# Kernel optimization log

Hardware: AMD Instinct MI355X
Metric: run time of the kernel (lower is better)

The kernel has to match this reference:

```python
import jax, jax.numpy as jnp
import numpy as np

WINDOW_SIZE = 11
SIGMA = 1.5
COLOR_TRANS = np.array([65.738, 129.057, 25.064], dtype=np.float32)
C1 = (0.01 * 255) ** 2
C2 = (0.03 * 255) ** 2


def _make_window(ws=WINDOW_SIZE, sigma=SIGMA):
    x = np.arange(ws, dtype=np.float32)
    g = np.exp(-((x - ws // 2) ** 2) / (2.0 * sigma ** 2))
    g = g / g.sum()
    w2d = np.outer(g, g).astype(np.float32)  # [ws, ws]
    return jnp.asarray(w2d[None, None])      # [1,1,ws,ws] OIHW


def _conv(x, w):
    # x: [B,1,H,W], w: [1,1,ws,ws], VALID padding, single channel
    return jax.lax.conv_general_dilated(
        x, w, window_strides=(1, 1), padding='VALID',
        dimension_numbers=('NCHW', 'OIHW', 'NCHW'))


def _luma(img):
    # img: [B,H,W,>=3] in [-1,1] -> [B,1,H,W] luma in [16,235]-ish
    rgb = (img[..., :3] + 1.0) / 2.0 * 255.0
    y = jnp.matmul(rgb, jnp.asarray(COLOR_TRANS)) / 256.0 + 16.0
    return y[:, None, :, :]


def setup_inputs() -> dict:
    key = jax.random.key(0)
    k1, k2 = jax.random.split(key)
    shape = (32, 512, 512, 3)
    img1 = jax.random.uniform(k1, shape, jnp.float32, -1.0, 1.0)
    img2 = jax.random.uniform(k2, shape, jnp.float32, -1.0, 1.0)
    return {"img1": img1, "img2": img2}


def reference(img1, img2):
    w = _make_window()
    x1 = _luma(img1)
    x2 = _luma(img2)
    mu1 = _conv(x1, w)
    mu2 = _conv(x2, w)
    mu1_sq = mu1 * mu1
    mu2_sq = mu2 * mu2
    mu1_mu2 = mu1 * mu2
    sigma1_sq = _conv(x1 * x1, w) - mu1_sq
    sigma2_sq = _conv(x2 * x2, w) - mu2_sq
    sigma12 = _conv(x1 * x2, w) - mu1_mu2
    ssim_map = ((2 * mu1_mu2 + C1) * (2 * sigma12 + C2)) / (
        (mu1_sq + mu2_sq + C1) * (sigma1_sq + sigma2_sq + C2))
    return jnp.mean(ssim_map)
```

## Files before the change

kernel.cpp:

```cpp
#include <hip/hip_runtime.h>
#include <math.h>

#define BATCH 32
#define H 512
#define W 512
#define OUTD 502
#define WS 11
#define TX 32
#define TY 32
#define IX 42
#define IY 42

#define C1F 6.5025f
#define C2F 58.5225f
#define N_OUT_TOTAL 8064128.0

struct GW { float g[WS]; };

__global__ __launch_bounds__(256) void ssim_tile_kernel(
    const float* __restrict__ img1, const float* __restrict__ img2,
    double* __restrict__ acc, GW w)
{
    __shared__ float sA[IY][IX + 2];
    __shared__ float sB[IY][IX + 2];
    __shared__ float hc[5][IY][TX + 1];
    __shared__ double wsum[4];

    const int tid  = threadIdx.x;
    const int c0   = blockIdx.x * TX;
    const int r0   = blockIdx.y * TY;
    const int b    = blockIdx.z;

    {
        const int tx = tid & 63;
        const int ty = tid >> 6;
        if (tx < IX) {
            const int col = c0 + tx;
            for (int iy = ty; iy < IY; iy += 4) {
                const int row = r0 + iy;
                float la = 0.f, lb = 0.f;
                if (row < H && col < W) {
                    const size_t base = ((size_t)(b * H + row) * W + col) * 3;
                    float r1 = img1[base], g1 = img1[base + 1], b1 = img1[base + 2];
                    float r2 = img2[base], g2 = img2[base + 1], b2 = img2[base + 2];
                    r1 = (r1 + 1.f) * 127.5f; g1 = (g1 + 1.f) * 127.5f; b1 = (b1 + 1.f) * 127.5f;
                    r2 = (r2 + 1.f) * 127.5f; g2 = (g2 + 1.f) * 127.5f; b2 = (b2 + 1.f) * 127.5f;
                    la = (r1 * 65.738f + g1 * 129.057f + b1 * 25.064f) * (1.f / 256.f) + 16.f;
                    lb = (r2 * 65.738f + g2 * 129.057f + b2 * 25.064f) * (1.f / 256.f) + 16.f;
                }
                sA[iy][tx] = la;
                sB[iy][tx] = lb;
            }
        }
    }
    __syncthreads();

    {
        const int ox = tid & 31;
        const int ty = tid >> 5;
        for (int iy = ty; iy < IY; iy += 8) {
            float s0 = 0.f, s1 = 0.f, s2 = 0.f, s3 = 0.f, s4 = 0.f;
            #pragma unroll
            for (int k = 0; k < WS; ++k) {
                const float gk = w.g[k];
                const float a = sA[iy][ox + k];
                const float c = sB[iy][ox + k];
                s0 += gk * a;
                s1 += gk * c;
                s2 += gk * a * a;
                s3 += gk * c * c;
                s4 += gk * a * c;
            }
            hc[0][iy][ox] = s0;
            hc[1][iy][ox] = s1;
            hc[2][iy][ox] = s2;
            hc[3][iy][ox] = s3;
            hc[4][iy][ox] = s4;
        }
    }
    __syncthreads();

    double local = 0.0;
    {
        const int ox = tid & 31;
        const int ty = tid >> 5;
        const bool col_ok = (c0 + ox) < OUTD;
        for (int oy = ty; oy < TY; oy += 8) {
            if (col_ok && (r0 + oy) < OUTD) {
                float mu1 = 0.f, mu2 = 0.f, e11 = 0.f, e22 = 0.f, e12 = 0.f;
                #pragma unroll
                for (int k = 0; k < WS; ++k) {
                    const float gk = w.g[k];
                    mu1 += gk * hc[0][oy + k][ox];
                    mu2 += gk * hc[1][oy + k][ox];
                    e11 += gk * hc[2][oy + k][ox];
                    e22 += gk * hc[3][oy + k][ox];
                    e12 += gk * hc[4][oy + k][ox];
                }
                const float mu1s = mu1 * mu1;
                const float mu2s = mu2 * mu2;
                const float mu12 = mu1 * mu2;
                const float s1q = e11 - mu1s;
                const float s2q = e22 - mu2s;
                const float s12 = e12 - mu12;
                const float num = (2.f * mu12 + C1F) * (2.f * s12 + C2F);
                const float den = (mu1s + mu2s + C1F) * (s1q + s2q + C2F);
                local += (double)(num / den);
            }
        }
    }

    for (int off = 32; off > 0; off >>= 1)
        local += __shfl_down(local, off, 64);
    const int lane = tid & 63;
    const int wv   = tid >> 6;
    if (lane == 0) wsum[wv] = local;
    __syncthreads();
    if (tid == 0) {
        const double t = wsum[0] + wsum[1] + wsum[2] + wsum[3];
        atomicAdd(acc, t);
    }
}

__global__ void ssim_finalize_kernel(const double* __restrict__ acc,
                                     float* __restrict__ out)
{
    out[0] = (float)(acc[0] / N_OUT_TOTAL);
}

extern "C" void kernel_launch(void* const* d_in, const int* in_sizes, int n_in,
                              void* d_out, int out_size, void* d_ws, size_t ws_size,
                              hipStream_t stream) {
    const float* img1 = (const float*)d_in[0];
    const float* img2 = (const float*)d_in[1];
    float* out = (float*)d_out;
    double* acc = (double*)d_ws;

    GW w;
    {
        float g[WS];
        float s = 0.f;
        for (int i = 0; i < WS; ++i) {
            const float x = (float)(i - WS / 2);
            g[i] = expf(-(x * x) / (2.f * 1.5f * 1.5f));
            s += g[i];
        }
        for (int i = 0; i < WS; ++i) w.g[i] = g[i] / s;
    }

    hipMemsetAsync(d_ws, 0, sizeof(double), stream);

    dim3 grid((OUTD + TX - 1) / TX, (OUTD + TY - 1) / TY, BATCH);
    ssim_tile_kernel<<<grid, 256, 0, stream>>>(img1, img2, acc, w);
    ssim_finalize_kernel<<<1, 1, 0, stream>>>(acc, out);
}
```

Measured before the change: 303.1 us.

## Stream rows through double-buffered LDS with register-resident vertical accumulators

Replaces the 32x32 2D tile kernel with a strip kernel where each thread owns one output column across a 32-row strip. Input rows are loaded one at a time into a double-buffered LDS row and prefetched a row ahead. The horizontal pass runs per row, and its result is scattered into an 11-deep ring of register accumulators for the vertical pass. This cuts the LDS footprint and the horizontal halo recompute (256-wide columns instead of 32). In exchange it adds a barrier per row, heavy register use (55 accumulators), and fewer blocks with wide column tiles.

```diff
diff --git a/kernel.cpp b/kernel.cpp
--- a/kernel.cpp
+++ b/kernel.cpp
@@ -6,119 +6,180 @@
 #define W 512
 #define OUTD 502
 #define WS 11
-#define TX 32
-#define TY 32
-#define IX 42
-#define IY 42
+#define STRIP 32
+#define INROWS 42
+#define BW 266
 
 #define C1F 6.5025f
 #define C2F 58.5225f
 #define N_OUT_TOTAL 8064128.0
 
 struct GW { float g[WS]; };
-
-__global__ __launch_bounds__(256) void ssim_tile_kernel(
+struct H5 { float v[5]; };
+
+__global__ __launch_bounds__(256, 4) void ssim_stream_kernel(
     const float* __restrict__ img1, const float* __restrict__ img2,
-    double* __restrict__ acc, GW w)
+    double* __restrict__ acc_out, GW wv)
 {
-    __shared__ float sA[IY][IX + 2];
-    __shared__ float sB[IY][IX + 2];
-    __shared__ float hc[5][IY][TX + 1];
+    __shared__ float bufA[2][BW];
+    __shared__ float bufB[2][BW];
     __shared__ double wsum[4];
 
-    const int tid  = threadIdx.x;
-    const int c0   = blockIdx.x * TX;
-    const int r0   = blockIdx.y * TY;
-    const int b    = blockIdx.z;
+    const int t  = threadIdx.x;
+    const int bx = blockIdx.x;
+    const int by = blockIdx.y;
+    const int b  = blockIdx.z;
+
+    const int c0   = bx * 256;
+    const int ox   = c0 + t;
+    const int r0   = by * STRIP;
+    const bool colok = (ox < OUTD);
+
+    const size_t imgbase = (size_t)b * H * W * 3;
+
+    auto load_luma = [&](int iy, float& la, float& lb, float& la2, float& lb2) {
+        la = lb = la2 = lb2 = 0.f;
+        const int r = r0 + iy;
+        if (iy < INROWS && r < H) {
+            const size_t rowb = imgbase + (size_t)r * (W * 3);
+            {
+                const size_t p = rowb + (size_t)(c0 + t) * 3;
+                float r1 = img1[p], g1 = img1[p + 1], b1 = img1[p + 2];
+                float r2 = img2[p], g2 = img2[p + 1], b2 = img2[p + 2];
+                r1 = (r1 + 1.f) * 127.5f; g1 = (g1 + 1.f) * 127.5f; b1 = (b1 + 1.f) * 127.5f;
+                r2 = (r2 + 1.f) * 127.5f; g2 = (g2 + 1.f) * 127.5f; b2 = (b2 + 1.f) * 127.5f;
+                la = (r1 * 65.738f + g1 * 129.057f + b1 * 25.064f) * (1.f / 256.f) + 16.f;
+                lb = (r2 * 65.738f + g2 * 129.057f + b2 * 25.064f) * (1.f / 256.f) + 16.f;
+            }
+            if (t < 10 && (c0 + 256 + t) < W) {
+                const size_t p = rowb + (size_t)(c0 + 256 + t) * 3;
+                float r1 = img1[p], g1 = img1[p + 1], b1 = img1[p + 2];
+                float r2 = img2[p], g2 = img2[p + 1], b2 = img2[p + 2];
+                r1 = (r1 + 1.f) * 127.5f; g1 = (g1 + 1.f) * 127.5f; b1 = (b1 + 1.f) * 127.5f;
+                r2 = (r2 + 1.f) * 127.5f; g2 = (g2 + 1.f) * 127.5f; b2 = (b2 + 1.f) * 127.5f;
+                la2 = (r1 * 65.738f + g1 * 129.057f + b1 * 25.064f) * (1.f / 256.f) + 16.f;
+                lb2 = (r2 * 65.738f + g2 * 129.057f + b2 * 25.064f) * (1.f / 256.f) + 16.f;
+            }
+        }
+    };
+
+    float rlA, rlB, rlA2, rlB2;
 
     {
-        const int tx = tid & 63;
-        const int ty = tid >> 6;
-        if (tx < IX) {
-            const int col = c0 + tx;
-            for (int iy = ty; iy < IY; iy += 4) {
-                const int row = r0 + iy;
-                float la = 0.f, lb = 0.f;
-                if (row < H && col < W) {
-                    const size_t base = ((size_t)(b * H + row) * W + col) * 3;
-                    float r1 = img1[base], g1 = img1[base + 1], b1 = img1[base + 2];
-                    float r2 = img2[base], g2 = img2[base + 1], b2 = img2[base + 2];
-                    r1 = (r1 + 1.f) * 127.5f; g1 = (g1 + 1.f) * 127.5f; b1 = (b1 + 1.f) * 127.5f;
-                    r2 = (r2 + 1.f) * 127.5f; g2 = (g2 + 1.f) * 127.5f; b2 = (b2 + 1.f) * 127.5f;
-                    la = (r1 * 65.738f + g1 * 129.057f + b1 * 25.064f) * (1.f / 256.f) + 16.f;
-                    lb = (r2 * 65.738f + g2 * 129.057f + b2 * 25.064f) * (1.f / 256.f) + 16.f;
-                }
-                sA[iy][tx] = la;
-                sB[iy][tx] = lb;
-            }
-        }
-    }
-    __syncthreads();
-
-    {
-        const int ox = tid & 31;
-        const int ty = tid >> 5;
-        for (int iy = ty; iy < IY; iy += 8) {
-            float s0 = 0.f, s1 = 0.f, s2 = 0.f, s3 = 0.f, s4 = 0.f;
+        float a, bv, a2, b2;
+        load_luma(0, a, bv, a2, b2);
+        load_luma(1, rlA, rlB, rlA2, rlB2);
+        bufA[0][t] = a; bufB[0][t] = bv;
+        if (t < 10) { bufA[0][256 + t] = a2; bufB[0][256 + t] = b2; }
+    }
+
+    auto row_step = [&](int iy) -> H5 {
+        float nA, nB, nA2, nB2;
+        load_luma(iy + 2, nA, nB, nA2, nB2);
+        __syncthreads();
+        {
+            const int wb = (iy + 1) & 1;
+            bufA[wb][t] = rlA; bufB[wb][t] = rlB;
+            if (t < 10) { bufA[wb][256 + t] = rlA2; bufB[wb][256 + t] = rlB2; }
+        }
+        rlA = nA; rlB = nB; rlA2 = nA2; rlB2 = nB2;
+        const float* __restrict__ ra = bufA[iy & 1];
+        const float* __restrict__ rb = bufB[iy & 1];
+        float h0 = 0.f, h1 = 0.f, h2 = 0.f, h3 = 0.f, h4 = 0.f;
+        #pragma unroll
+        for (int k = 0; k < WS; ++k) {
+            const float gk = wv.g[k];
+            const float a = ra[t + k];
+            const float c = rb[t + k];
+            h0 += gk * a;
+            h1 += gk * c;
+            h2 += gk * a * a;
+            h3 += gk * c * c;
+            h4 += gk * a * c;
+        }
+        H5 h; h.v[0] = h0; h.v[1] = h1; h.v[2] = h2; h.v[3] = h3; h.v[4] = h4;
+        return h;
+    };
+
+    double local = 0.0;
+    auto complete = [&](const float* a, int oy) {
+        if (colok && (r0 + oy) < OUTD) {
+            const float mu1 = a[0], mu2 = a[1];
+            const float mu1s = mu1 * mu1, mu2s = mu2 * mu2, mu12 = mu1 * mu2;
+            const float num = (2.f * mu12 + C1F) * (2.f * (a[4] - mu12) + C2F);
+            const float den = (mu1s + mu2s + C1F) * ((a[2] - mu1s) + (a[3] - mu2s) + C2F);
+            local += (double)(num / den);
+        }
+    };
+
+    float acc[WS][5];
+    #pragma unroll
+    for (int s = 0; s < WS; ++s)
+        #pragma unroll
+        for (int ch = 0; ch < 5; ++ch) acc[s][ch] = 0.f;
+
+    #pragma unroll
+    for (int j = 0; j < 11; ++j) {
+        H5 h = row_step(j);
+        #pragma unroll
+        for (int k = 0; k < WS; ++k) {
+            if (k <= j) {
+                const float gk = wv.g[k];
+                #pragma unroll
+                for (int ch = 0; ch < 5; ++ch) acc[j - k][ch] += gk * h.v[ch];
+            }
+        }
+    }
+    complete(acc[0], 0);
+    #pragma unroll
+    for (int ch = 0; ch < 5; ++ch) acc[0][ch] = 0.f;
+
+    for (int c = 1; c <= 2; ++c) {
+        const int iy0 = c * 11;
+        #pragma unroll
+        for (int j = 0; j < 11; ++j) {
+            H5 h = row_step(iy0 + j);
             #pragma unroll
             for (int k = 0; k < WS; ++k) {
-                const float gk = w.g[k];
-                const float a = sA[iy][ox + k];
-                const float c = sB[iy][ox + k];
-                s0 += gk * a;
-                s1 += gk * c;
-                s2 += gk * a * a;
-                s3 += gk * c * c;
-                s4 += gk * a * c;
-            }
-            hc[0][iy][ox] = s0;
-            hc[1][iy][ox] = s1;
-            hc[2][iy][ox] = s2;
-            hc[3][iy][ox] = s3;
-            hc[4][iy][ox] = s4;
-        }
-    }
-    __syncthreads();
-
-    double local = 0.0;
-    {
-        const int ox = tid & 31;
-        const int ty = tid >> 5;
-        const bool col_ok = (c0 + ox) < OUTD;
-        for (int oy = ty; oy < TY; oy += 8) {
-            if (col_ok && (r0 + oy) < OUTD) {
-                float mu1 = 0.f, mu2 = 0.f, e11 = 0.f, e22 = 0.f, e12 = 0.f;
+                const float gk = wv.g[k];
+                const int s = (j - k + 11) % 11;
                 #pragma unroll
-                for (int k = 0; k < WS; ++k) {
-                    const float gk = w.g[k];
-                    mu1 += gk * hc[0][oy + k][ox];
-                    mu2 += gk * hc[1][oy + k][ox];
-                    e11 += gk * hc[2][oy + k][ox];
-                    e22 += gk * hc[3][oy + k][ox];
-                    e12 += gk * hc[4][oy + k][ox];
-                }
-                const float mu1s = mu1 * mu1;
-                const float mu2s = mu2 * mu2;
-                const float mu12 = mu1 * mu2;
-                const float s1q = e11 - mu1s;
-                const float s2q = e22 - mu2s;
-                const float s12 = e12 - mu12;
-                const float num = (2.f * mu12 + C1F) * (2.f * s12 + C2F);
-                const float den = (mu1s + mu2s + C1F) * (s1q + s2q + C2F);
-                local += (double)(num / den);
-            }
-        }
+                for (int ch = 0; ch < 5; ++ch) acc[s][ch] += gk * h.v[ch];
+            }
+            const int sc = (j + 1) % 11;
+            complete(acc[sc], iy0 + j - 10);
+            #pragma unroll
+            for (int ch = 0; ch < 5; ++ch) acc[sc][ch] = 0.f;
+        }
+    }
+
+    #pragma unroll
+    for (int j = 0; j < 9; ++j) {
+        H5 h = row_step(33 + j);
+        #pragma unroll
+        for (int k = 0; k < WS; ++k) {
+            if (k >= j + 2) {
+                const float gk = wv.g[k];
+                const int s = (j - k + 22) % 11;
+                #pragma unroll
+                for (int ch = 0; ch < 5; ++ch) acc[s][ch] += gk * h.v[ch];
+            }
+        }
+        const int sc = (j + 1) % 11;
+        complete(acc[sc], 23 + j);
+        #pragma unroll
+        for (int ch = 0; ch < 5; ++ch) acc[sc][ch] = 0.f;
     }
 
     for (int off = 32; off > 0; off >>= 1)
         local += __shfl_down(local, off, 64);
-    const int lane = tid & 63;
-    const int wv   = tid >> 6;
-    if (lane == 0) wsum[wv] = local;
+    const int lane = t & 63;
+    const int wvid = t >> 6;
+    if (lane == 0) wsum[wvid] = local;
     __syncthreads();
-    if (tid == 0) {
-        const double t = wsum[0] + wsum[1] + wsum[2] + wsum[3];
-        atomicAdd(acc, t);
+    if (t == 0) {
+        const double s = wsum[0] + wsum[1] + wsum[2] + wsum[3];
+        atomicAdd(acc_out, s);
     }
 }
 
@@ -150,7 +211,7 @@
 
     hipMemsetAsync(d_ws, 0, sizeof(double), stream);
 
-    dim3 grid((OUTD + TX - 1) / TX, (OUTD + TY - 1) / TY, BATCH);
-    ssim_tile_kernel<<<grid, 256, 0, stream>>>(img1, img2, acc, w);
+    dim3 grid(2, (OUTD + STRIP - 1) / STRIP, BATCH);
+    ssim_stream_kernel<<<grid, 256, 0, stream>>>(img1, img2, acc, w);
     ssim_finalize_kernel<<<1, 1, 0, stream>>>(acc, out);
 }
```

After: 311.6 us. +2.8%, slower.

## Stream rows through registers with ring-buffered vertical Gaussian pass

Applied to the files above, without the earlier changes.

Replaces the 32x32 2D tile kernel with a row-streaming kernel. Each thread owns one output column of a 256-wide strip, computes horizontal sums per input row from a double-buffered shared row, and keeps 11 rows of horizontal results in registers for the vertical pass. The x1^2 and x2^2 channels are merged into a single sum since only their total is used. This cuts the halo recompute and shared-memory traffic of the 2D tiles, at the cost of a __syncthreads per row, high register use, fewer blocks, and column loads strided by three floats.

```diff
diff --git a/kernel.cpp b/kernel.cpp
--- a/kernel.cpp
+++ b/kernel.cpp
@@ -6,10 +6,9 @@
 #define W 512
 #define OUTD 502
 #define WS 11
-#define TX 32
-#define TY 32
-#define IX 42
-#define IY 42
+#define STRIP 32
+#define INROWS 42
+#define BW 266
 
 #define C1F 6.5025f
 #define C2F 58.5225f
@@ -17,108 +16,147 @@
 
 struct GW { float g[WS]; };
 
-__global__ __launch_bounds__(256) void ssim_tile_kernel(
+__device__ __forceinline__ float luma3(float r, float g, float b) {
+    r = (r + 1.f) * 127.5f; g = (g + 1.f) * 127.5f; b = (b + 1.f) * 127.5f;
+    return (r * 65.738f + g * 129.057f + b * 25.064f) * (1.f / 256.f) + 16.f;
+}
+
+__global__ __launch_bounds__(256) void ssim_stream_kernel(
     const float* __restrict__ img1, const float* __restrict__ img2,
-    double* __restrict__ acc, GW w)
+    double* __restrict__ acc_out, GW wv)
 {
-    __shared__ float sA[IY][IX + 2];
-    __shared__ float sB[IY][IX + 2];
-    __shared__ float hc[5][IY][TX + 1];
+    __shared__ float bufA[2][BW];
+    __shared__ float bufB[2][BW];
     __shared__ double wsum[4];
 
-    const int tid  = threadIdx.x;
-    const int c0   = blockIdx.x * TX;
-    const int r0   = blockIdx.y * TY;
-    const int b    = blockIdx.z;
+    const int t  = threadIdx.x;
+    const int bx = blockIdx.x;
+    const int by = blockIdx.y;
+    const int b  = blockIdx.z;
+
+    const int c0 = bx * 256;
+    const int ox = c0 + t;
+    const int r0 = by * STRIP;
+    const bool colok = (ox < OUTD);
+    const bool halo  = (t < 10) && ((c0 + 256 + t) < W);
+    const size_t imgbase = (size_t)b * (H * W * 3);
+    const size_t colA = (size_t)(c0 + t) * 3;
+    const size_t colB = (size_t)(c0 + 256 + t) * 3;
+
+    float rlA, rlB, rlA2, rlB2;
+    float nA, nB, nA2, nB2;
+
+#define LOAD_LUMA(IY, LA, LB, LA2, LB2)                                   \
+    {                                                                     \
+        LA = LB = LA2 = LB2 = 0.f;                                        \
+        const int _r = r0 + (IY);                                         \
+        if ((IY) < INROWS && _r < H) {                                    \
+            const size_t _rowb = imgbase + (size_t)_r * (W * 3);          \
+            {                                                             \
+                const float* _p1 = img1 + _rowb + colA;                   \
+                const float* _p2 = img2 + _rowb + colA;                   \
+                LA = luma3(_p1[0], _p1[1], _p1[2]);                       \
+                LB = luma3(_p2[0], _p2[1], _p2[2]);                       \
+            }                                                             \
+            if (halo) {                                                   \
+                const float* _p1 = img1 + _rowb + colB;                   \
+                const float* _p2 = img2 + _rowb + colB;                   \
+                LA2 = luma3(_p1[0], _p1[1], _p1[2]);                      \
+                LB2 = luma3(_p2[0], _p2[1], _p2[2]);                      \
+            }                                                             \
+        }                                                                 \
+    }
+
+    float rm1[WS], rm2[WS], rq[WS], rx[WS];
 
     {
-        const int tx = tid & 63;
-        const int ty = tid >> 6;
-        if (tx < IX) {
-            const int col = c0 + tx;
-            for (int iy = ty; iy < IY; iy += 4) {
-                const int row = r0 + iy;
-                float la = 0.f, lb = 0.f;
-                if (row < H && col < W) {
-                    const size_t base = ((size_t)(b * H + row) * W + col) * 3;
-                    float r1 = img1[base], g1 = img1[base + 1], b1 = img1[base + 2];
-                    float r2 = img2[base], g2 = img2[base + 1], b2 = img2[base + 2];
-                    r1 = (r1 + 1.f) * 127.5f; g1 = (g1 + 1.f) * 127.5f; b1 = (b1 + 1.f) * 127.5f;
-                    r2 = (r2 + 1.f) * 127.5f; g2 = (g2 + 1.f) * 127.5f; b2 = (b2 + 1.f) * 127.5f;
-                    la = (r1 * 65.738f + g1 * 129.057f + b1 * 25.064f) * (1.f / 256.f) + 16.f;
-                    lb = (r2 * 65.738f + g2 * 129.057f + b2 * 25.064f) * (1.f / 256.f) + 16.f;
-                }
-                sA[iy][tx] = la;
-                sB[iy][tx] = lb;
-            }
-        }
+        float a0, b0, a02, b02;
+        LOAD_LUMA(0, a0, b0, a02, b02);
+        LOAD_LUMA(1, rlA, rlB, rlA2, rlB2);
+        bufA[0][t] = a0; bufB[0][t] = b0;
+        if (t < 10) { bufA[0][256 + t] = a02; bufB[0][256 + t] = b02; }
     }
-    __syncthreads();
 
-    {
-        const int ox = tid & 31;
-        const int ty = tid >> 5;
-        for (int iy = ty; iy < IY; iy += 8) {
-            float s0 = 0.f, s1 = 0.f, s2 = 0.f, s3 = 0.f, s4 = 0.f;
-            #pragma unroll
-            for (int k = 0; k < WS; ++k) {
-                const float gk = w.g[k];
-                const float a = sA[iy][ox + k];
-                const float c = sB[iy][ox + k];
-                s0 += gk * a;
-                s1 += gk * c;
-                s2 += gk * a * a;
-                s3 += gk * c * c;
-                s4 += gk * a * c;
-            }
-            hc[0][iy][ox] = s0;
-            hc[1][iy][ox] = s1;
-            hc[2][iy][ox] = s2;
-            hc[3][iy][ox] = s3;
-            hc[4][iy][ox] = s4;
-        }
+#define ROW_STEP(IY, H0, H1, H2, H3)                                      \
+    {                                                                     \
+        LOAD_LUMA((IY) + 2, nA, nB, nA2, nB2);                            \
+        __syncthreads();                                                  \
+        {                                                                 \
+            const int _wb = ((IY) + 1) & 1;                               \
+            bufA[_wb][t] = rlA; bufB[_wb][t] = rlB;                       \
+            if (t < 10) { bufA[_wb][256 + t] = rlA2;                      \
+                          bufB[_wb][256 + t] = rlB2; }                    \
+        }                                                                 \
+        rlA = nA; rlB = nB; rlA2 = nA2; rlB2 = nB2;                       \
+        {                                                                 \
+            const int _rbidx = (IY) & 1;                                  \
+            float _h0 = 0.f, _h1 = 0.f, _h2 = 0.f, _h3 = 0.f;             \
+            _Pragma("unroll")                                             \
+            for (int _k = 0; _k < WS; ++_k) {                             \
+                const float _gk = wv.g[_k];                               \
+                const float _a = bufA[_rbidx][t + _k];                    \
+                const float _c = bufB[_rbidx][t + _k];                    \
+                _h0 += _gk * _a;                                          \
+                _h1 += _gk * _c;                                          \
+                _h2 += _gk * (_a * _a + _c * _c);                         \
+                _h3 += _gk * (_a * _c);                                   \
+            }                                                             \
+            H0 = _h0; H1 = _h1; H2 = _h2; H3 = _h3;                       \
+        }                                                                 \
     }
-    __syncthreads();
+
+    #pragma unroll
+    for (int j = 0; j < 10; ++j)
+        ROW_STEP(j, rm1[j], rm2[j], rq[j], rx[j]);
 
     double local = 0.0;
-    {
-        const int ox = tid & 31;
-        const int ty = tid >> 5;
-        const bool col_ok = (c0 + ox) < OUTD;
-        for (int oy = ty; oy < TY; oy += 8) {
-            if (col_ok && (r0 + oy) < OUTD) {
-                float mu1 = 0.f, mu2 = 0.f, e11 = 0.f, e22 = 0.f, e12 = 0.f;
-                #pragma unroll
-                for (int k = 0; k < WS; ++k) {
-                    const float gk = w.g[k];
-                    mu1 += gk * hc[0][oy + k][ox];
-                    mu2 += gk * hc[1][oy + k][ox];
-                    e11 += gk * hc[2][oy + k][ox];
-                    e22 += gk * hc[3][oy + k][ox];
-                    e12 += gk * hc[4][oy + k][ox];
-                }
-                const float mu1s = mu1 * mu1;
-                const float mu2s = mu2 * mu2;
-                const float mu12 = mu1 * mu2;
-                const float s1q = e11 - mu1s;
-                const float s2q = e22 - mu2s;
-                const float s12 = e12 - mu12;
-                const float num = (2.f * mu12 + C1F) * (2.f * s12 + C2F);
-                const float den = (mu1s + mu2s + C1F) * (s1q + s2q + C2F);
-                local += (double)(num / den);
-            }
-        }
+
+#define DO_ROW(OY, JM)                                                    \
+    {                                                                     \
+        ROW_STEP((OY) + 10,                                               \
+                 rm1[((JM) + 10) % WS], rm2[((JM) + 10) % WS],            \
+                 rq[((JM) + 10) % WS],  rx[((JM) + 10) % WS]);            \
+        float _mu1 = 0.f, _mu2 = 0.f, _eq = 0.f, _ex = 0.f;               \
+        _Pragma("unroll")                                                 \
+        for (int _k = 0; _k < WS; ++_k) {                                 \
+            const float _gk = wv.g[_k];                                   \
+            const int _s = ((JM) + _k) % WS;                              \
+            _mu1 += _gk * rm1[_s];                                        \
+            _mu2 += _gk * rm2[_s];                                        \
+            _eq  += _gk * rq[_s];                                         \
+            _ex  += _gk * rx[_s];                                         \
+        }                                                                 \
+        if (colok && (r0 + (OY)) < OUTD) {                                \
+            const float _m1s = _mu1 * _mu1;                               \
+            const float _m2s = _mu2 * _mu2;                               \
+            const float _m12 = _mu1 * _mu2;                               \
+            const float _num = (2.f * _m12 + C1F) *                       \
+                               (2.f * (_ex - _m12) + C2F);                \
+            const float _den = (_m1s + _m2s + C1F) *                      \
+                               ((_eq - _m1s - _m2s) + C2F);               \
+            local += (double)(_num / _den);                               \
+        }                                                                 \
     }
+
+    for (int c = 0; c < 2; ++c) {
+        const int base = c * 11;
+        #pragma unroll
+        for (int j = 0; j < 11; ++j)
+            DO_ROW(base + j, j);
+    }
+    #pragma unroll
+    for (int j = 0; j < 10; ++j)
+        DO_ROW(22 + j, j);
 
     for (int off = 32; off > 0; off >>= 1)
         local += __shfl_down(local, off, 64);
-    const int lane = tid & 63;
-    const int wv   = tid >> 6;
-    if (lane == 0) wsum[wv] = local;
+    const int lane = t & 63;
+    const int wvid = t >> 6;
+    if (lane == 0) wsum[wvid] = local;
     __syncthreads();
-    if (tid == 0) {
-        const double t = wsum[0] + wsum[1] + wsum[2] + wsum[3];
-        atomicAdd(acc, t);
+    if (t == 0) {
+        const double s = wsum[0] + wsum[1] + wsum[2] + wsum[3];
+        atomicAdd(acc_out, s);
     }
 }
 
@@ -150,7 +188,7 @@
 
     hipMemsetAsync(d_ws, 0, sizeof(double), stream);
 
-    dim3 grid((OUTD + TX - 1) / TX, (OUTD + TY - 1) / TY, BATCH);
-    ssim_tile_kernel<<<grid, 256, 0, stream>>>(img1, img2, acc, w);
+    dim3 grid(2, (OUTD + STRIP - 1) / STRIP, BATCH);
+    ssim_stream_kernel<<<grid, 256, 0, stream>>>(img1, img2, acc, w);
     ssim_finalize_kernel<<<1, 1, 0, stream>>>(acc, out);
 }
```

Result: faster. 275.0 us (-9.3%).
